# Kernel optimization log

Measured on AMD Instinct MI355X. Metric: run time of the kernel, lower is better.

The kernel has to match this reference:

```python
import jax, jax.numpy as jnp
import numpy as np

C_M, C, C_Z = 64, 32, 128
LN_EPS = 1e-5


def setup_inputs() -> dict:
    key = jax.random.key(0)
    ks = jax.random.split(key, 6)
    S, N = 128, 384
    msa_feat = jax.random.normal(ks[0], (S, N, C_M), dtype=jnp.float32)
    msa_mask = jnp.ones((S, N), dtype=jnp.float32)
    # LayerNorm params
    ln_gamma = jnp.ones((C_M,), dtype=jnp.float32)
    ln_beta = jnp.zeros((C_M,), dtype=jnp.float32)
    # Linear weights stored as [in, out] (jax convention)
    w_a = jax.random.normal(ks[1], (C_M, C), dtype=jnp.float32) / np.sqrt(C_M)
    w_b = jax.random.normal(ks[2], (C_M, C), dtype=jnp.float32) / np.sqrt(C_M)
    w_out = jax.random.normal(ks[3], (C * C, C_Z), dtype=jnp.float32) / np.sqrt(C * C)
    b_out = jnp.zeros((C_Z,), dtype=jnp.float32)
    return {"msa_feat": msa_feat, "msa_mask": msa_mask, "ln_gamma": ln_gamma,
            "ln_beta": ln_beta, "w_a": w_a, "w_b": w_b, "w_out": w_out, "b_out": b_out}


def _layer_norm(x, gamma, beta):
    mu = jnp.mean(x, axis=-1, keepdims=True)
    var = jnp.mean(jnp.square(x - mu), axis=-1, keepdims=True)
    return (x - mu) * jax.lax.rsqrt(var + LN_EPS) * gamma + beta


def reference(msa_feat, msa_mask, ln_gamma, ln_beta, w_a, w_b, w_out, b_out):
    # msa_feat: [S, N, c_m], msa_mask: [S, N]
    m = _layer_norm(msa_feat, ln_gamma, ln_beta)
    m_a = jnp.einsum('snm,mc->snc', m, w_a) * msa_mask[..., None]  # [S, N, c]
    m_b = jnp.einsum('snm,mc->snc', m, w_b) * msa_mask[..., None]  # [S, N, c]
    ab = jnp.einsum('sic,sjd->ijcd', m_a, m_b)                     # [N, N, c, c]
    N = ab.shape[0]
    ab = ab.reshape(N, N, C * C)
    z = jnp.einsum('ijk,kz->ijz', ab, w_out) + b_out               # [N, N, c_z]
    norm = jnp.einsum('si,sj->ij', msa_mask, msa_mask)             # [N, N]
    z = z / (norm[..., None] + 0.001)
    return z
```

## Files before the change

kernel.cpp:

```cpp
#include <hip/hip_runtime.h>
#include <hip/hip_bf16.h>

#define S_DIM 128
#define N_PTS 384
#define CM    64
#define C_DIM 32
#define CZ    128
#define NC    (N_PTS*C_DIM)

typedef __attribute__((ext_vector_type(8)))  __bf16 bf16x8;
typedef __attribute__((ext_vector_type(16))) float  f32x16;
typedef unsigned short u16;
typedef unsigned int   u32;

__device__ __forceinline__ bf16x8 lds_frag(const void* base, int byteoff){
  union { uint4 u; bf16x8 v; } x;
  x.u = *(const uint4*)((const char*)base + byteoff);
  return x.v;
}
__device__ __forceinline__ u32 pk2(float a, float b){
  __hip_bfloat162 h;
  h.x = (__hip_bfloat16)a;
  h.y = (__hip_bfloat16)b;
  union { __hip_bfloat162 h2; u32 u; } c; c.h2 = h;
  return c.u;
}

__global__ __launch_bounds__(512) void k_prep(
    const float* __restrict__ msa, const float* __restrict__ mask,
    const float* __restrict__ gamma, const float* __restrict__ beta,
    const float* __restrict__ wa, const float* __restrict__ wb,
    const float* __restrict__ w_out,
    __hip_bfloat16* __restrict__ A_ws, __hip_bfloat16* __restrict__ B_ws,
    __hip_bfloat16* __restrict__ wt, float* __restrict__ nrm_g){
  __shared__ union {
    u16   X[128*64];
    float T[64*128];
  } sh;
  __shared__ float ln_mk[128];

  const int bid = blockIdx.x, tid = threadIdx.x;

  if (bid >= 640){
    int i = bid - 640, j = tid;
    if (j < N_PTS){
      float a = 0.f;
      #pragma unroll 8
      for (int s = 0; s < S_DIM; ++s)
        a += mask[s*N_PTS + i] * mask[s*N_PTS + j];
      nrm_g[i*N_PTS + j] = a;
    }
    return;
  }
  if (bid >= 384){
    int o = (bid - 384)*512 + tid;
    int z = o >> 10, mi = o & 1023;
    int e = mi & 7, j = (mi >> 3) & 3, hi = (mi >> 5) & 1, Q = mi >> 6;
    int ks = Q*4 + j;
    int pos = ks*16 + hi*8 + e;
    int c = ((pos >> 7) << 2) | (pos & 3);
    int d = (pos >> 2) & 31;
    int k = c*32 + d;
    wt[o] = (__hip_bfloat16)w_out[k*CZ + z];
    return;
  }

  const int w = tid >> 6, l = tid & 63;
  const int hi = l >> 5, ln = l & 31;
  const int n = bid;

  if (tid < 128) ln_mk[tid] = mask[tid*N_PTS + n];

  const float g  = gamma[l];
  const float be = beta[l];

  #pragma unroll
  for (int t = 0; t < 16; ++t){
    int s = w*16 + t;
    float x = msa[((size_t)s*N_PTS + n)*CM + l];
    float sum = x;
    #pragma unroll
    for (int m = 1; m < 64; m <<= 1) sum += __shfl_xor(sum, m, 64);
    float mu = sum * (1.0f/64.0f);
    float dx = x - mu;
    float vs = dx*dx;
    #pragma unroll
    for (int m = 1; m < 64; m <<= 1) vs += __shfl_xor(vs, m, 64);
    float rstd = rsqrtf(vs*(1.0f/64.0f) + 1e-5f);
    float xn = dx*rstd*g + be;
    __hip_bfloat16 hx = (__hip_bfloat16)xn;
    *(u16*)((char*)sh.X + s*128 + ((l*2) ^ ((s&7)<<4))) = *(u16*)&hx;
  }
  __syncthreads();

  const int mb = w >> 1, mat = w & 1;
  const float* W = mat ? wb : wa;
  f32x16 pacc;
  #pragma unroll
  for (int r = 0; r < 16; ++r) pacc[r] = 0.f;
  #pragma unroll
  for (int ks = 0; ks < 4; ++ks){
    int srow = mb*32 + ln;
    bf16x8 aF = lds_frag(sh.X, srow*128 + (((ks*32 + hi*16)) ^ ((srow&7)<<4)));
    union { u32 u[4]; bf16x8 v; } bx;
    #pragma unroll
    for (int e = 0; e < 4; ++e){
      int m = ks*16 + hi*8 + e*2;
      bx.u[e] = pk2(W[m*C_DIM + ln], W[(m+1)*C_DIM + ln]);
    }
    pacc = __builtin_amdgcn_mfma_f32_32x32x16_bf16(aF, bx.v, pacc, 0, 0, 0);
  }
  __syncthreads();

  const int col = mat*32 + ln;
  #pragma unroll
  for (int r = 0; r < 16; ++r){
    int rr = (r & 3) + ((r >> 2) << 3) + (hi << 2);
    int s = mb*32 + rr;
    *(float*)((char*)sh.T + col*512 + ((s*4) ^ ((col&7)<<4))) = pacc[r] * ln_mk[s];
  }
  __syncthreads();

  {
    int col2 = tid >> 3, sc = tid & 7;
    __hip_bfloat16* O = (col2 < 32) ? A_ws : B_ws;
    int row = n*C_DIM + (col2 & 31);
    uint4 pk_0, pk_1;
    u32* pw0 = (u32*)&pk_0;
    u32* pw1 = (u32*)&pk_1;
    #pragma unroll
    for (int q = 0; q < 4; ++q){
      union { uint4 u4; float f[4]; } rd;
      rd.u4 = *(const uint4*)((const char*)sh.T + col2*512 + ((sc*64 + q*16) ^ ((col2&7)<<4)));
      u32 a = pk2(rd.f[0], rd.f[1]);
      u32 b = pk2(rd.f[2], rd.f[3]);
      if (q < 2){ pw0[q*2] = a; pw0[q*2+1] = b; }
      else      { pw1[(q-2)*2] = a; pw1[(q-2)*2+1] = b; }
    }
    int swz = (row & 15) << 4;
    *(uint4*)((char*)O + (size_t)row*256 + ((sc*32)      ^ swz)) = pk_0;
    *(uint4*)((char*)O + (size_t)row*256 + ((sc*32 + 16) ^ swz)) = pk_1;
  }
}

__global__ __launch_bounds__(512, 2) void k_fused(
    const __hip_bfloat16* __restrict__ A_ws, const __hip_bfloat16* __restrict__ B_ws,
    const __hip_bfloat16* __restrict__ Wt,  const float* __restrict__ b_out,
    const float* __restrict__ nrm_g, float* __restrict__ out){
  __shared__ union {
    struct { u16 A[256*128]; u16 B[256*128]; } s1;
    struct { u16 P[64*1024]; } s2;
  } sh;
  __shared__ float nrm[64];

  const int tid = threadIdx.x;
  const int w = tid >> 6, l = tid & 63;
  const int hi = l >> 5, ln = l & 31;
  const int bi = blockIdx.x, bj = blockIdx.y;

  char* shA = (char*)sh.s1.A;
  char* shB = (char*)sh.s1.B;
  const char* Ag = (const char*)A_ws + (size_t)bi*65536;
  const char* Bg = (const char*)B_ws + (size_t)bj*65536;
  #pragma unroll
  for (int it = 0; it < 8; ++it){
    int o = (it*512 + tid) * 16;
    *(uint4*)(shA + o) = *(const uint4*)(Ag + o);
    *(uint4*)(shB + o) = *(const uint4*)(Bg + o);
  }

  if (tid < 64){
    int i = bi*8 + (tid >> 3), jj = bj*8 + (tid & 7);
    nrm[tid] = nrm_g[i*N_PTS + jj];
  }
  const int kh = w >> 2, cc = w & 3;
  const char* wbase = (const char*)Wt + (size_t)(cc*32 + ln)*2048 + kh*1024 + hi*64;
  uint4 wreg[16];
  #pragma unroll
  for (int u = 0; u < 8; ++u)
    wreg[u] = *(const uint4*)(wbase + (u>>2)*128 + (u&3)*16);
  __syncthreads();

  const int wr = w >> 2, wc = w & 3;
  f32x16 acc[4][2];
  #pragma unroll
  for (int mb = 0; mb < 4; ++mb)
    #pragma unroll
    for (int nb = 0; nb < 2; ++nb)
      #pragma unroll
      for (int r = 0; r < 16; ++r) acc[mb][nb][r] = 0.f;

  #pragma unroll
  for (int ks = 0; ks < 8; ++ks){
    const int k0b = ks*32 + hi*16;
    bf16x8 aF[4], bF[2];
    #pragma unroll
    for (int mb = 0; mb < 4; ++mb){
      int m = wr*128 + mb*32 + ln;
      aF[mb] = lds_frag(shA, m*256 + (k0b ^ ((m & 15) << 4)));
    }
    #pragma unroll
    for (int nb = 0; nb < 2; ++nb){
      int n = wc*64 + nb*32 + ln;
      bF[nb] = lds_frag(shB, n*256 + (k0b ^ ((n & 15) << 4)));
    }
    #pragma unroll
    for (int mb = 0; mb < 4; ++mb)
      #pragma unroll
      for (int nb = 0; nb < 2; ++nb)
        acc[mb][nb] = __builtin_amdgcn_mfma_f32_32x32x16_bf16(aF[mb], bF[nb], acc[mb][nb], 0, 0, 0);
  }
  __syncthreads();

  char* shP = (char*)sh.s2.P;
  #pragma unroll
  for (int u = 8; u < 16; ++u)
    wreg[u] = *(const uint4*)(wbase + (u>>2)*128 + (u&3)*16);
  #pragma unroll
  for (int mb = 0; mb < 4; ++mb)
    #pragma unroll
    for (int nb = 0; nb < 2; ++nb){
      int p = (wr*4 + mb)*8 + (wc*2 + nb);
      int base = p*2048, sw = (p & 15) << 4;
      #pragma unroll
      for (int g = 0; g < 4; ++g){
        uint2 v;
        v.x = pk2(acc[mb][nb][4*g + 0], acc[mb][nb][4*g + 1]);
        v.y = pk2(acc[mb][nb][4*g + 2], acc[mb][nb][4*g + 3]);
        int off = ((2*g + hi)*256 + ln*8) ^ sw;
        *(uint2*)(shP + base + off) = v;
      }
    }
  __syncthreads();

  f32x16 zc0, zc1;
  #pragma unroll
  for (int r = 0; r < 16; ++r){ zc0[r] = 0.f; zc1[r] = 0.f; }

  const char* prow0 = shP + (size_t)ln*2048;
  const char* prow1 = shP + (size_t)(32 + ln)*2048;
  const int sw2 = (ln & 15) << 4;
  const int kbase = kh*1024;

  #pragma unroll
  for (int rd = 0; rd < 8; ++rd){
    bf16x8 a0[4], a1[4];
    #pragma unroll
    for (int u = 0; u < 4; ++u){
      int off = (kbase + (rd*4 + u)*32 + hi*16) ^ sw2;
      a0[u] = lds_frag(prow0, off);
      a1[u] = lds_frag(prow1, off);
    }
    __builtin_amdgcn_s_setprio(1);
    #pragma unroll
    for (int u = 0; u < 4; ++u){
      union { uint4 q; bf16x8 v; } bx; bx.q = wreg[(rd & 3)*4 + u];
      zc0 = __builtin_amdgcn_mfma_f32_32x32x16_bf16(a0[u], bx.v, zc0, 0, 0, 0);
      zc1 = __builtin_amdgcn_mfma_f32_32x32x16_bf16(a1[u], bx.v, zc1, 0, 0, 0);
    }
    __builtin_amdgcn_s_setprio(0);
    if (rd < 4){
      #pragma unroll
      for (int u = 0; u < 4; ++u)
        wreg[(rd & 3)*4 + u] = *(const uint4*)(wbase + (rd + 4)*128 + u*16);
    }
  }
  __syncthreads();

  float* red0 = (float*)sh.s2.P;
  float* red1 = (float*)sh.s2.P + 32*128;
  if (kh == 0){
    #pragma unroll
    for (int r = 0; r < 16; ++r){
      int pr = (r & 3) + ((r >> 2) << 3) + (hi << 2);
      red1[pr*128 + cc*32 + ln] = zc1[r];
    }
  } else {
    #pragma unroll
    for (int r = 0; r < 16; ++r){
      int pr = (r & 3) + ((r >> 2) << 3) + (hi << 2);
      red0[pr*128 + cc*32 + ln] = zc0[r];
    }
  }
  __syncthreads();
  {
    const int z = cc*32 + ln;
    const float bo = b_out[z];
    if (kh == 0){
      #pragma unroll
      for (int r = 0; r < 16; ++r){
        int pr = (r & 3) + ((r >> 2) << 3) + (hi << 2);
        float v = (zc0[r] + red0[pr*128 + z] + bo) / (nrm[pr] + 0.001f);
        int i = bi*8 + (pr >> 3), j = bj*8 + (pr & 7);
        out[((size_t)i*N_PTS + j)*CZ + z] = v;
      }
    } else {
      #pragma unroll
      for (int r = 0; r < 16; ++r){
        int pr = (r & 3) + ((r >> 2) << 3) + (hi << 2);
        int p = 32 + pr;
        float v = (zc1[r] + red1[pr*128 + z] + bo) / (nrm[p] + 0.001f);
        int i = bi*8 + (p >> 3), j = bj*8 + (p & 7);
        out[((size_t)i*N_PTS + j)*CZ + z] = v;
      }
    }
  }
}

extern "C" void kernel_launch(void* const* d_in, const int* in_sizes, int n_in,
                              void* d_out, int out_size, void* d_ws, size_t ws_size,
                              hipStream_t stream) {
  (void)in_sizes; (void)n_in; (void)out_size; (void)ws_size;
  const float* msa   = (const float*)d_in[0];
  const float* mask  = (const float*)d_in[1];
  const float* gamma = (const float*)d_in[2];
  const float* beta  = (const float*)d_in[3];
  const float* wa    = (const float*)d_in[4];
  const float* wb    = (const float*)d_in[5];
  const float* wout  = (const float*)d_in[6];
  const float* bout  = (const float*)d_in[7];

  __hip_bfloat16* A_ws = (__hip_bfloat16*)d_ws;
  __hip_bfloat16* B_ws = A_ws + (size_t)NC*S_DIM;
  __hip_bfloat16* Wt   = B_ws + (size_t)NC*S_DIM;
  float* nrm_g = (float*)(Wt + (size_t)CZ*1024);
  float* outp  = (float*)d_out;

  k_prep<<<1024, 512, 0, stream>>>(msa, mask, gamma, beta, wa, wb, wout,
                                   A_ws, B_ws, Wt, nrm_g);
  dim3 g2(48, 48, 1);
  k_fused<<<g2, 512, 0, stream>>>(A_ws, B_ws, Wt, bout, nrm_g, outp);
}
```

Baseline: 127.5 us.

## Make fused kernel persistent with register prefetch of next B tile

Replaces the 48x48 grid with 256 persistent blocks, each handling 9 consecutive (i,j) tiles in a loop. The next B tile is prefetched into registers partway through the second GEMM so its global load overlaps compute. This removes block launch and ramp overhead, but adds register pressure from the pfB array and extra barriers per iteration. The A tile is still reloaded from global on every iteration.

```diff
diff --git a/kernel.cpp b/kernel.cpp
--- a/kernel.cpp
+++ b/kernel.cpp
@@ -156,154 +156,177 @@
   const int tid = threadIdx.x;
   const int w = tid >> 6, l = tid & 63;
   const int hi = l >> 5, ln = l & 31;
-  const int bi = blockIdx.x, bj = blockIdx.y;
+  const int kh = w >> 2, cc = w & 3;
+  const int wr = w >> 2, wc = w & 3;
+  const int b = blockIdx.x;
 
   char* shA = (char*)sh.s1.A;
   char* shB = (char*)sh.s1.B;
-  const char* Ag = (const char*)A_ws + (size_t)bi*65536;
-  const char* Bg = (const char*)B_ws + (size_t)bj*65536;
-  #pragma unroll
-  for (int it = 0; it < 8; ++it){
-    int o = (it*512 + tid) * 16;
-    *(uint4*)(shA + o) = *(const uint4*)(Ag + o);
-    *(uint4*)(shB + o) = *(const uint4*)(Bg + o);
-  }
-
-  if (tid < 64){
-    int i = bi*8 + (tid >> 3), jj = bj*8 + (tid & 7);
-    nrm[tid] = nrm_g[i*N_PTS + jj];
-  }
-  const int kh = w >> 2, cc = w & 3;
+  char* shP = (char*)sh.s2.P;
+
   const char* wbase = (const char*)Wt + (size_t)(cc*32 + ln)*2048 + kh*1024 + hi*64;
-  uint4 wreg[16];
-  #pragma unroll
-  for (int u = 0; u < 8; ++u)
-    wreg[u] = *(const uint4*)(wbase + (u>>2)*128 + (u&3)*16);
-  __syncthreads();
-
-  const int wr = w >> 2, wc = w & 3;
-  f32x16 acc[4][2];
-  #pragma unroll
-  for (int mb = 0; mb < 4; ++mb)
-    #pragma unroll
-    for (int nb = 0; nb < 2; ++nb)
-      #pragma unroll
-      for (int r = 0; r < 16; ++r) acc[mb][nb][r] = 0.f;
-
-  #pragma unroll
-  for (int ks = 0; ks < 8; ++ks){
-    const int k0b = ks*32 + hi*16;
-    bf16x8 aF[4], bF[2];
-    #pragma unroll
-    for (int mb = 0; mb < 4; ++mb){
-      int m = wr*128 + mb*32 + ln;
-      aF[mb] = lds_frag(shA, m*256 + (k0b ^ ((m & 15) << 4)));
-    }
-    #pragma unroll
-    for (int nb = 0; nb < 2; ++nb){
-      int n = wc*64 + nb*32 + ln;
-      bF[nb] = lds_frag(shB, n*256 + (k0b ^ ((n & 15) << 4)));
-    }
-    #pragma unroll
-    for (int mb = 0; mb < 4; ++mb)
-      #pragma unroll
-      for (int nb = 0; nb < 2; ++nb)
-        acc[mb][nb] = __builtin_amdgcn_mfma_f32_32x32x16_bf16(aF[mb], bF[nb], acc[mb][nb], 0, 0, 0);
-  }
-  __syncthreads();
-
-  char* shP = (char*)sh.s2.P;
-  #pragma unroll
-  for (int u = 8; u < 16; ++u)
-    wreg[u] = *(const uint4*)(wbase + (u>>2)*128 + (u&3)*16);
-  #pragma unroll
-  for (int mb = 0; mb < 4; ++mb)
-    #pragma unroll
-    for (int nb = 0; nb < 2; ++nb){
-      int p = (wr*4 + mb)*8 + (wc*2 + nb);
-      int base = p*2048, sw = (p & 15) << 4;
-      #pragma unroll
-      for (int g = 0; g < 4; ++g){
-        uint2 v;
-        v.x = pk2(acc[mb][nb][4*g + 0], acc[mb][nb][4*g + 1]);
-        v.y = pk2(acc[mb][nb][4*g + 2], acc[mb][nb][4*g + 3]);
-        int off = ((2*g + hi)*256 + ln*8) ^ sw;
-        *(uint2*)(shP + base + off) = v;
-      }
-    }
-  __syncthreads();
-
-  f32x16 zc0, zc1;
-  #pragma unroll
-  for (int r = 0; r < 16; ++r){ zc0[r] = 0.f; zc1[r] = 0.f; }
-
+  const float bo = b_out[cc*32 + ln];
+  const int sw2 = (ln & 15) << 4;
+  const int kbase = kh*1024;
   const char* prow0 = shP + (size_t)ln*2048;
   const char* prow1 = shP + (size_t)(32 + ln)*2048;
-  const int sw2 = (ln & 15) << 4;
-  const int kbase = kh*1024;
-
-  #pragma unroll
-  for (int rd = 0; rd < 8; ++rd){
-    bf16x8 a0[4], a1[4];
-    #pragma unroll
-    for (int u = 0; u < 4; ++u){
-      int off = (kbase + (rd*4 + u)*32 + hi*16) ^ sw2;
-      a0[u] = lds_frag(prow0, off);
-      a1[u] = lds_frag(prow1, off);
-    }
-    __builtin_amdgcn_s_setprio(1);
-    #pragma unroll
-    for (int u = 0; u < 4; ++u){
-      union { uint4 q; bf16x8 v; } bx; bx.q = wreg[(rd & 3)*4 + u];
-      zc0 = __builtin_amdgcn_mfma_f32_32x32x16_bf16(a0[u], bx.v, zc0, 0, 0, 0);
-      zc1 = __builtin_amdgcn_mfma_f32_32x32x16_bf16(a1[u], bx.v, zc1, 0, 0, 0);
-    }
-    __builtin_amdgcn_s_setprio(0);
-    if (rd < 4){
-      #pragma unroll
-      for (int u = 0; u < 4; ++u)
-        wreg[(rd & 3)*4 + u] = *(const uint4*)(wbase + (rd + 4)*128 + u*16);
-    }
-  }
-  __syncthreads();
-
-  float* red0 = (float*)sh.s2.P;
-  float* red1 = (float*)sh.s2.P + 32*128;
-  if (kh == 0){
-    #pragma unroll
-    for (int r = 0; r < 16; ++r){
-      int pr = (r & 3) + ((r >> 2) << 3) + (hi << 2);
-      red1[pr*128 + cc*32 + ln] = zc1[r];
-    }
-  } else {
-    #pragma unroll
-    for (int r = 0; r < 16; ++r){
-      int pr = (r & 3) + ((r >> 2) << 3) + (hi << 2);
-      red0[pr*128 + cc*32 + ln] = zc0[r];
-    }
-  }
-  __syncthreads();
+
+  uint4 pfB[8];
   {
-    const int z = cc*32 + ln;
-    const float bo = b_out[z];
+    const char* Bg = (const char*)B_ws + (size_t)((b*9) % 48)*65536;
+    #pragma unroll
+    for (int q = 0; q < 8; ++q) pfB[q] = *(const uint4*)(Bg + (q*512 + tid)*16);
+  }
+  uint4 wreg[16];
+
+  #pragma unroll 1
+  for (int it = 0; it < 9; ++it){
+    const int t = b*9 + it;
+    const int bi = t/48, bj = t%48;
+
+    const char* Ag = (const char*)A_ws + (size_t)bi*65536;
+    uint4 tA[8];
+    #pragma unroll
+    for (int q = 0; q < 8; ++q) tA[q] = *(const uint4*)(Ag + (q*512 + tid)*16);
+    #pragma unroll
+    for (int q = 0; q < 8; ++q)
+      *(uint4*)(shB + (q*512 + tid)*16) = pfB[q];
+    #pragma unroll
+    for (int q = 0; q < 8; ++q)
+      *(uint4*)(shA + (q*512 + tid)*16) = tA[q];
+
+    if (tid < 64){
+      int i = bi*8 + (tid >> 3), jj = bj*8 + (tid & 7);
+      nrm[tid] = nrm_g[i*N_PTS + jj];
+    }
+    #pragma unroll
+    for (int u = 0; u < 8; ++u)
+      wreg[u] = *(const uint4*)(wbase + (u>>2)*128 + (u&3)*16);
+    __syncthreads();
+
+    f32x16 acc[4][2];
+    #pragma unroll
+    for (int mb = 0; mb < 4; ++mb)
+      #pragma unroll
+      for (int nb = 0; nb < 2; ++nb)
+        #pragma unroll
+        for (int r = 0; r < 16; ++r) acc[mb][nb][r] = 0.f;
+
+    #pragma unroll
+    for (int ks = 0; ks < 8; ++ks){
+      const int k0b = ks*32 + hi*16;
+      bf16x8 aF[4], bF[2];
+      #pragma unroll
+      for (int mb = 0; mb < 4; ++mb){
+        int m = wr*128 + mb*32 + ln;
+        aF[mb] = lds_frag(shA, m*256 + (k0b ^ ((m & 15) << 4)));
+      }
+      #pragma unroll
+      for (int nb = 0; nb < 2; ++nb){
+        int n = wc*64 + nb*32 + ln;
+        bF[nb] = lds_frag(shB, n*256 + (k0b ^ ((n & 15) << 4)));
+      }
+      #pragma unroll
+      for (int mb = 0; mb < 4; ++mb)
+        #pragma unroll
+        for (int nb = 0; nb < 2; ++nb)
+          acc[mb][nb] = __builtin_amdgcn_mfma_f32_32x32x16_bf16(aF[mb], bF[nb], acc[mb][nb], 0, 0, 0);
+    }
+    __syncthreads();
+
+    #pragma unroll
+    for (int u = 8; u < 16; ++u)
+      wreg[u] = *(const uint4*)(wbase + (u>>2)*128 + (u&3)*16);
+    #pragma unroll
+    for (int mb = 0; mb < 4; ++mb)
+      #pragma unroll
+      for (int nb = 0; nb < 2; ++nb){
+        int p = (wr*4 + mb)*8 + (wc*2 + nb);
+        int base = p*2048, sw = (p & 15) << 4;
+        #pragma unroll
+        for (int g = 0; g < 4; ++g){
+          uint2 v;
+          v.x = pk2(acc[mb][nb][4*g + 0], acc[mb][nb][4*g + 1]);
+          v.y = pk2(acc[mb][nb][4*g + 2], acc[mb][nb][4*g + 3]);
+          int off = ((2*g + hi)*256 + ln*8) ^ sw;
+          *(uint2*)(shP + base + off) = v;
+        }
+      }
+    __syncthreads();
+
+    f32x16 zc0, zc1;
+    #pragma unroll
+    for (int r = 0; r < 16; ++r){ zc0[r] = 0.f; zc1[r] = 0.f; }
+
+    #pragma unroll
+    for (int rd = 0; rd < 8; ++rd){
+      bf16x8 a0[4], a1[4];
+      #pragma unroll
+      for (int u = 0; u < 4; ++u){
+        int off = (kbase + (rd*4 + u)*32 + hi*16) ^ sw2;
+        a0[u] = lds_frag(prow0, off);
+        a1[u] = lds_frag(prow1, off);
+      }
+      __builtin_amdgcn_s_setprio(1);
+      #pragma unroll
+      for (int u = 0; u < 4; ++u){
+        union { uint4 q; bf16x8 v; } bx; bx.q = wreg[(rd & 3)*4 + u];
+        zc0 = __builtin_amdgcn_mfma_f32_32x32x16_bf16(a0[u], bx.v, zc0, 0, 0, 0);
+        zc1 = __builtin_amdgcn_mfma_f32_32x32x16_bf16(a1[u], bx.v, zc1, 0, 0, 0);
+      }
+      __builtin_amdgcn_s_setprio(0);
+      if (rd < 4){
+        #pragma unroll
+        for (int u = 0; u < 4; ++u)
+          wreg[(rd & 3)*4 + u] = *(const uint4*)(wbase + (rd + 4)*128 + u*16);
+      }
+      if (rd == 3 && it < 8){
+        const char* Bg2 = (const char*)B_ws + (size_t)((t + 1) % 48)*65536;
+        #pragma unroll
+        for (int q = 0; q < 8; ++q)
+          pfB[q] = *(const uint4*)(Bg2 + (q*512 + tid)*16);
+      }
+    }
+    __syncthreads();
+
+    float* red0 = (float*)sh.s2.P;
+    float* red1 = (float*)sh.s2.P + 32*128;
     if (kh == 0){
       #pragma unroll
       for (int r = 0; r < 16; ++r){
         int pr = (r & 3) + ((r >> 2) << 3) + (hi << 2);
-        float v = (zc0[r] + red0[pr*128 + z] + bo) / (nrm[pr] + 0.001f);
-        int i = bi*8 + (pr >> 3), j = bj*8 + (pr & 7);
-        out[((size_t)i*N_PTS + j)*CZ + z] = v;
+        red1[pr*128 + cc*32 + ln] = zc1[r];
       }
     } else {
       #pragma unroll
       for (int r = 0; r < 16; ++r){
         int pr = (r & 3) + ((r >> 2) << 3) + (hi << 2);
-        int p = 32 + pr;
-        float v = (zc1[r] + red1[pr*128 + z] + bo) / (nrm[p] + 0.001f);
-        int i = bi*8 + (p >> 3), j = bj*8 + (p & 7);
-        out[((size_t)i*N_PTS + j)*CZ + z] = v;
-      }
-    }
+        red0[pr*128 + cc*32 + ln] = zc0[r];
+      }
+    }
+    __syncthreads();
+    {
+      const int z = cc*32 + ln;
+      if (kh == 0){
+        #pragma unroll
+        for (int r = 0; r < 16; ++r){
+          int pr = (r & 3) + ((r >> 2) << 3) + (hi << 2);
+          float v = (zc0[r] + red0[pr*128 + z] + bo) / (nrm[pr] + 0.001f);
+          int i = bi*8 + (pr >> 3), j = bj*8 + (pr & 7);
+          out[((size_t)i*N_PTS + j)*CZ + z] = v;
+        }
+      } else {
+        #pragma unroll
+        for (int r = 0; r < 16; ++r){
+          int pr = (r & 3) + ((r >> 2) << 3) + (hi << 2);
+          int p = 32 + pr;
+          float v = (zc1[r] + red1[pr*128 + z] + bo) / (nrm[p] + 0.001f);
+          int i = bi*8 + (p >> 3), j = bj*8 + (p & 7);
+          out[((size_t)i*N_PTS + j)*CZ + z] = v;
+        }
+      }
+    }
+    __syncthreads();
   }
 }
 
@@ -328,6 +351,5 @@
 
   k_prep<<<1024, 512, 0, stream>>>(msa, mask, gamma, beta, wa, wb, wout,
                                    A_ws, B_ws, Wt, nrm_g);
-  dim3 g2(48, 48, 1);
-  k_fused<<<g2, 512, 0, stream>>>(A_ws, B_ws, Wt, bout, nrm_g, outp);
-}
+  k_fused<<<256, 512, 0, stream>>>(A_ws, B_ws, Wt, bout, nrm_g, outp);
+}
```

New measurement: 335.6 us. 163% more time.
